# Kernel tuning notes

Measured on AMD Instinct MI355X. Metric: run time of the kernel, lower is better.

Reference implementation:

```python
import jax, jax.numpy as jnp
import numpy as np

N_NODES = 50000
N_EDGES = 800000
N_GRAPHS = 128
IN_DIM = 12          # state_ndim + action_ndim
C = 64               # n_channels
N_LAYERS = 2
NEG_SLOPE = 0.01     # torch leaky_relu default


def setup_inputs() -> dict:
    key = jax.random.key(0)
    ks = jax.random.split(key, 16)
    state = jax.random.normal(ks[0], (N_NODES, 8), dtype=jnp.float32)
    action = jax.random.normal(ks[1], (N_NODES, 4), dtype=jnp.float32)
    edge_index = jax.random.randint(ks[2], (2, N_EDGES), 0, N_NODES, dtype=jnp.int64)
    edge_attr = jax.random.normal(ks[3], (N_EDGES, IN_DIM), dtype=jnp.float32)
    batch = jnp.sort(jax.random.randint(ks[4], (N_NODES,), 0, N_GRAPHS, dtype=jnp.int64))
    s = 0.05
    params = {
        "W_in": jax.random.normal(ks[5], (IN_DIM, C), dtype=jnp.float32) * s,
        "b_in": jnp.zeros((C,), dtype=jnp.float32),
        "W_self": jax.random.normal(ks[6], (N_LAYERS, C, C), dtype=jnp.float32) * s,
        "W_nbr": jax.random.normal(ks[7], (N_LAYERS, C, C), dtype=jnp.float32) * s,
        "W_edge": jax.random.normal(ks[8], (N_LAYERS, IN_DIM, C), dtype=jnp.float32) * s,
        "b_conv": jnp.zeros((N_LAYERS, C), dtype=jnp.float32),
        "W_out": jax.random.normal(ks[9], (C, 1), dtype=jnp.float32) * s,
        "b_out": jnp.zeros((1,), dtype=jnp.float32),
    }
    return {"state": state, "action": action, "edge_index": edge_index,
            "edge_attr": edge_attr, "batch": batch, **params}


def reference(state, action, edge_index, edge_attr, batch,
              W_in, b_in, W_self, W_nbr, W_edge, b_conv, W_out, b_out):
    N = state.shape[0]
    src, dst = edge_index[0], edge_index[1]
    act = lambda v: jax.nn.leaky_relu(v, NEG_SLOPE)

    # read-in: concat state/action -> node embedding [N, C]
    x = jnp.concatenate([state, action], axis=-1)
    h = act(x @ W_in + b_in)

    # message passing: gather -> transform -> scatter-add, edge_attr-conditioned
    for l in range(W_self.shape[0]):
        m = h[src] @ W_nbr[l] + edge_attr @ W_edge[l]          # [E, C]
        agg = jax.ops.segment_sum(m, dst, num_segments=N)      # [N, C]
        h = act(h @ W_self[l] + agg + b_conv[l])

    # read-out to scalar per node, then scatter_mean over graph ids
    y = h @ W_out + b_out                                      # [N, 1]
    sums = jax.ops.segment_sum(y, batch, num_segments=N_GRAPHS)
    counts = jax.ops.segment_sum(jnp.ones((N, 1), y.dtype), batch,
                                 num_segments=N_GRAPHS)
    return sums / jnp.maximum(counts, 1.0)                     # [B, 1]
```

## Files before the change

kernel.cpp:

```cpp
#include <hip/hip_runtime.h>

#define NN 50000
#define NE 800000
#define NG 128
#define IN_DIM 12
#define C 64
#define NEG_SLOPE 0.01f
#define SCAN_BLOCKS 196

typedef short short8 __attribute__((ext_vector_type(8)));
typedef float f32x4 __attribute__((ext_vector_type(4)));
typedef unsigned int uint4v __attribute__((ext_vector_type(4)));

__device__ __forceinline__ float lrelu(float v) {
    return v > 0.f ? v : NEG_SLOPE * v;
}
__device__ __forceinline__ float bflo(uint32_t v) { return __uint_as_float(v << 16); }
__device__ __forceinline__ float bfhi(uint32_t v) { return __uint_as_float(v & 0xffff0000u); }
__device__ __forceinline__ unsigned short bf16r(float x) {
    uint32_t u = __float_as_uint(x);
    u += 0x7fffu + ((u >> 16) & 1u);
    return (unsigned short)(u >> 16);
}
__device__ __forceinline__ uint32_t pack_bf16(float lo, float hi) {
    return (uint32_t)bf16r(lo) | ((uint32_t)bf16r(hi) << 16);
}

__global__ void readin_kernel(const float* __restrict__ state,
                              const float* __restrict__ action,
                              const float* __restrict__ W_in,
                              const float* __restrict__ b_in,
                              uint32_t* __restrict__ hb) {
    __shared__ float sW[IN_DIM * C];
    __shared__ float sb[C];
    int tid = threadIdx.x;
    for (int i = tid; i < IN_DIM * C; i += blockDim.x) sW[i] = W_in[i];
    if (tid < C) sb[tid] = b_in[tid];
    __syncthreads();

    int node = blockIdx.x * (blockDim.x >> 6) + (tid >> 6);
    int c = tid & 63;
    if (node >= NN) return;

    float x[IN_DIM];
#pragma unroll
    for (int k = 0; k < 8; k++) x[k] = state[node * 8 + k];
#pragma unroll
    for (int k = 0; k < 4; k++) x[8 + k] = action[node * 4 + k];

    float acc = sb[c];
#pragma unroll
    for (int k = 0; k < IN_DIM; k++) acc += x[k] * sW[k * C + c];
    float res = lrelu(acc);
    float p = __shfl_xor(res, 1);
    if (!(c & 1)) hb[node * 32 + (c >> 1)] = pack_bf16(res, p);
}

__global__ void hist_kernel(const int* __restrict__ dst, int* __restrict__ deg) {
    int e = blockIdx.x * blockDim.x + threadIdx.x;
    if (e < NE) atomicAdd(&deg[dst[e]], 1);
}

__global__ void scan1_kernel(const int* __restrict__ deg,
                             int* __restrict__ excl,
                             int* __restrict__ bsum) {
    __shared__ int tmp[256];
    int tid = threadIdx.x;
    int i = blockIdx.x * 256 + tid;
    int v = (i < NN) ? deg[i] : 0;
    tmp[tid] = v;
    __syncthreads();
    for (int off = 1; off < 256; off <<= 1) {
        int t = (tid >= off) ? tmp[tid - off] : 0;
        __syncthreads();
        tmp[tid] += t;
        __syncthreads();
    }
    if (i < NN) excl[i] = tmp[tid] - v;
    if (tid == 255) bsum[blockIdx.x] = tmp[255];
}

__global__ void scan23_kernel(const int* __restrict__ excl,
                              const int* __restrict__ bsum,
                              int* __restrict__ row_start,
                              int* __restrict__ cursor) {
    __shared__ int s_off;
    int tid = threadIdx.x;
    if (tid < 64) {
        int p = 0;
        for (int i = tid; i < blockIdx.x; i += 64) p += bsum[i];
#pragma unroll
        for (int off = 32; off; off >>= 1) p += __shfl_xor(p, off);
        if (tid == 0) s_off = p;
    }
    __syncthreads();
    int i = blockIdx.x * 256 + tid;
    if (i < NN) {
        int v = excl[i] + s_off;
        row_start[i] = v;
        cursor[i] = v;
    }
}

__global__ void fill_kernel(const int* __restrict__ src,
                            const int* __restrict__ dst,
                            int* __restrict__ cursor,
                            int* __restrict__ csr_src,
                            int* __restrict__ csr_eid) {
    int e = blockIdx.x * blockDim.x + threadIdx.x;
    if (e >= NE) return;
    int d = dst[e];
    int slot = atomicAdd(&cursor[d], 1);
    csr_src[slot] = src[e];
    csr_eid[slot] = e;
}

__global__ void wprep_kernel(const float* __restrict__ W_self,
                             const float* __restrict__ W_nbr,
                             unsigned short* __restrict__ WT) {
    int idx = blockIdx.x * 256 + threadIdx.x;
    if (idx >= 2 * 64 * 128) return;
    int l = idx >> 13;
    int rem = idx & 8191;
    int col = rem >> 7;
    int k = rem & 127;
    float v = (k < C) ? W_self[l * C * C + k * C + col]
                      : W_nbr[l * C * C + (k - C) * C + col];
    WT[idx] = bf16r(v);
}

__global__ void agg_e_kernel(const float* __restrict__ edge_attr,
                             const int* __restrict__ row_start,
                             const int* __restrict__ deg,
                             const int* __restrict__ csr_eid,
                             const float* __restrict__ W_edge,
                             const float* __restrict__ b_conv,
                             float* __restrict__ E0,
                             float* __restrict__ E1) {
    __shared__ float sWe0[IN_DIM * C];
    __shared__ float sWe1[IN_DIM * C];
    __shared__ float sb0[C];
    __shared__ float sb1[C];
    int tid = threadIdx.x;
    for (int i = tid; i < IN_DIM * C; i += blockDim.x) {
        sWe0[i] = W_edge[i];
        sWe1[i] = W_edge[IN_DIM * C + i];
    }
    if (tid < C) { sb0[tid] = b_conv[tid]; sb1[tid] = b_conv[C + tid]; }
    __syncthreads();

    int node = blockIdx.x * (blockDim.x >> 6) + (tid >> 6);
    int lane = tid & 63;
    int g = lane >> 4;
    int cc = lane & 15;
    if (node >= NN) return;
    int start = row_start[node], cnt = deg[node];

    int myeid = (lane < cnt) ? csr_eid[start + lane] : 0;
    int nb = cnt < 64 ? cnt : 64;

    float acc = 0.f, acc2 = 0.f;
    int j = 0;
    for (; j + 8 <= nb; j += 8) {
        int e0 = __shfl(myeid, j + g);
        int e1 = __shfl(myeid, j + 4 + g);
        if (cc < IN_DIM) {
            acc  += edge_attr[e0 * IN_DIM + cc];
            acc2 += edge_attr[e1 * IN_DIM + cc];
        }
    }
    for (; j + 4 <= nb; j += 4) {
        int e0 = __shfl(myeid, j + g);
        if (cc < IN_DIM) acc += edge_attr[e0 * IN_DIM + cc];
    }
    {
        int e0 = __shfl(myeid, (j + g < 64) ? (j + g) : 0);
        if (j + g < nb && cc < IN_DIM) acc += edge_attr[e0 * IN_DIM + cc];
    }
    for (int i2 = 64 + g; i2 < cnt; i2 += 4) {
        int e = csr_eid[start + i2];
        if (cc < IN_DIM) acc += edge_attr[e * IN_DIM + cc];
    }
    acc += acc2;
    acc += __shfl_xor(acc, 16);
    acc += __shfl_xor(acc, 32);
    float e0v = sb0[lane];
    float e1v = sb1[lane];
#pragma unroll
    for (int k = 0; k < IN_DIM; k++) {
        float ak = __shfl(acc, k);
        e0v += ak * sWe0[k * C + lane];
        e1v += ak * sWe1[k * C + lane];
    }
    E0[node * C + lane] = e0v;
    E1[node * C + lane] = e1v;
}

__global__ void gather_kernel(const uint32_t* __restrict__ hb_in,
                              const int* __restrict__ row_start,
                              const int* __restrict__ deg,
                              const int* __restrict__ csr_src,
                              uint32_t* __restrict__ aggb) {
    int tid = threadIdx.x;
    int node = blockIdx.x * (blockDim.x >> 6) + (tid >> 6);
    int lane = tid & 63;
    if (node >= NN) return;

    int start = row_start[node], cnt = deg[node];
    int half = lane >> 5;
    int q = lane & 31;

    int myidx = (lane < cnt) ? csr_src[start + lane] : 0;
    int nb = cnt < 64 ? cnt : 64;

    float a0 = 0.f, a1 = 0.f, b0v = 0.f, b1v = 0.f;
    int j = 0;
    for (; j + 8 <= nb; j += 8) {
        int p = j + 4 * half;
        int s0 = __shfl(myidx, p);
        int s1 = __shfl(myidx, p + 1);
        int s2 = __shfl(myidx, p + 2);
        int s3 = __shfl(myidx, p + 3);
        uint32_t v0 = hb_in[s0 * 32 + q];
        uint32_t v1 = hb_in[s1 * 32 + q];
        uint32_t v2 = hb_in[s2 * 32 + q];
        uint32_t v3 = hb_in[s3 * 32 + q];
        a0  += bflo(v0); a1  += bfhi(v0);
        b0v += bflo(v1); b1v += bfhi(v1);
        a0  += bflo(v2); a1  += bfhi(v2);
        b0v += bflo(v3); b1v += bfhi(v3);
    }
    for (; j + 2 <= nb; j += 2) {
        int s = __shfl(myidx, j + half);
        uint32_t v = hb_in[s * 32 + q];
        a0 += bflo(v); a1 += bfhi(v);
    }
    {
        int s = __shfl(myidx, (j < 64) ? j : 0);
        if (j < nb && half == 0) {
            uint32_t v = hb_in[s * 32 + q];
            a0 += bflo(v); a1 += bfhi(v);
        }
    }
    for (int i2 = 64 + half; i2 < cnt; i2 += 2) {
        int s = csr_src[start + i2];
        uint32_t v = hb_in[s * 32 + q];
        a0 += bflo(v); a1 += bfhi(v);
    }
    a0 += b0v; a1 += b1v;
    a0 += __shfl_xor(a0, 32);
    a1 += __shfl_xor(a1, 32);
    if (lane < 32) aggb[node * 32 + q] = pack_bf16(a0, a1);
}

__global__ __launch_bounds__(512) void gemm_kernel(
        const uint32_t* __restrict__ hbA,
        const uint32_t* __restrict__ aggb,
        const unsigned short* __restrict__ WT,
        const float* __restrict__ E,
        unsigned short* __restrict__ hb_out) {
    int tid = threadIdx.x;
    int w = tid >> 6;
    int l = tid & 63;
    int mt = blockIdx.x * 2 + (w >> 2);
    if (mt * 16 >= NN) return;
    int nt = w & 3;
    int node_base = mt * 16;

    int arow = l & 15;
    int kg = l >> 4;
    int gcol = nt * 16 + arow;

    const uint32_t* aptr = hbA + (node_base + arow) * 32 + kg * 4;
    const uint32_t* gptr = aggb + (node_base + arow) * 32 + kg * 4;
    short8 a0 = __builtin_bit_cast(short8, *reinterpret_cast<const uint4v*>(aptr));
    short8 a1 = __builtin_bit_cast(short8, *reinterpret_cast<const uint4v*>(aptr + 16));
    short8 a2 = __builtin_bit_cast(short8, *reinterpret_cast<const uint4v*>(gptr));
    short8 a3 = __builtin_bit_cast(short8, *reinterpret_cast<const uint4v*>(gptr + 16));

    const unsigned short* bbase = WT + gcol * 128 + kg * 8;
    short8 b0 = __builtin_bit_cast(short8, *reinterpret_cast<const uint4v*>(bbase));
    short8 b1 = __builtin_bit_cast(short8, *reinterpret_cast<const uint4v*>(bbase + 32));
    short8 b2 = __builtin_bit_cast(short8, *reinterpret_cast<const uint4v*>(bbase + 64));
    short8 b3 = __builtin_bit_cast(short8, *reinterpret_cast<const uint4v*>(bbase + 96));

    f32x4 acc;
#pragma unroll
    for (int r = 0; r < 4; r++)
        acc[r] = E[(node_base + kg * 4 + r) * C + gcol];

    acc = __builtin_amdgcn_mfma_f32_16x16x32_bf16(a0, b0, acc, 0, 0, 0);
    acc = __builtin_amdgcn_mfma_f32_16x16x32_bf16(a1, b1, acc, 0, 0, 0);
    acc = __builtin_amdgcn_mfma_f32_16x16x32_bf16(a2, b2, acc, 0, 0, 0);
    acc = __builtin_amdgcn_mfma_f32_16x16x32_bf16(a3, b3, acc, 0, 0, 0);

#pragma unroll
    for (int r = 0; r < 4; r++) {
        float res = lrelu(acc[r]);
        hb_out[(node_base + kg * 4 + r) * C + gcol] = bf16r(res);
    }
}

__global__ void readout_fused(const unsigned short* __restrict__ hb,
                              const float* __restrict__ W_out,
                              const float* __restrict__ b_out,
                              const int* __restrict__ batch,
                              float* __restrict__ sums,
                              float* __restrict__ counts) {
    __shared__ float s_sum[NG];
    __shared__ float s_cnt[NG];
    int tid = threadIdx.x;
    if (tid < NG) { s_sum[tid] = 0.f; s_cnt[tid] = 0.f; }
    __syncthreads();

    int lane = tid & 63;
    int wave = tid >> 6;
    int base = blockIdx.x * 256 + wave * 64;
    float w = W_out[lane];
    float b0 = b_out[0];

    if (base < NN) {
        int last = base + 63;
        bool full = (last < NN);
        int gf = batch[base];
        int gl = batch[full ? last : (NN - 1)];
        if (full && gf == gl) {
            float p = 0.f;
            for (int i = 0; i < 64; i++)
                p += __uint_as_float((uint32_t)hb[(base + i) * C + lane] << 16);
            p *= w;
#pragma unroll
            for (int off = 32; off; off >>= 1) p += __shfl_xor(p, off);
            if (lane == 0) {
                atomicAdd(&s_sum[gf], p + 64.f * b0);
                atomicAdd(&s_cnt[gf], 64.f);
            }
        } else {
            float y_local = 0.f;
            for (int i = 0; i < 64; i++) {
                int nd = base + i;
                float v = 0.f;
                if (nd < NN) v = __uint_as_float((uint32_t)hb[nd * C + lane] << 16) * w;
#pragma unroll
                for (int off = 32; off; off >>= 1) v += __shfl_xor(v, off);
                if (lane == i) y_local = v + b0;
            }
            int nd = base + lane;
            if (nd < NN) {
                int g = batch[nd];
                atomicAdd(&s_sum[g], y_local);
                atomicAdd(&s_cnt[g], 1.0f);
            }
        }
    }
    __syncthreads();
    if (tid < NG && s_cnt[tid] != 0.f) {
        atomicAdd(&sums[tid], s_sum[tid]);
        atomicAdd(&counts[tid], s_cnt[tid]);
    }
}

__global__ void finalize_kernel(const float* __restrict__ sums,
                                const float* __restrict__ counts,
                                float* __restrict__ out) {
    int g = threadIdx.x;
    if (g < NG) out[g] = sums[g] / fmaxf(counts[g], 1.0f);
}

extern "C" void kernel_launch(void* const* d_in, const int* in_sizes, int n_in,
                              void* d_out, int out_size, void* d_ws, size_t ws_size,
                              hipStream_t stream) {
    const float* state     = (const float*)d_in[0];
    const float* action    = (const float*)d_in[1];
    const int*   edge_index= (const int*)d_in[2];
    const float* edge_attr = (const float*)d_in[3];
    const int*   batch     = (const int*)d_in[4];
    const float* W_in      = (const float*)d_in[5];
    const float* b_in      = (const float*)d_in[6];
    const float* W_self    = (const float*)d_in[7];
    const float* W_nbr     = (const float*)d_in[8];
    const float* W_edge    = (const float*)d_in[9];
    const float* b_conv    = (const float*)d_in[10];
    const float* W_out     = (const float*)d_in[11];
    const float* b_out     = (const float*)d_in[12];
    float* out = (float*)d_out;

    const int* src = edge_index;
    const int* dst = edge_index + NE;

    float* ws      = (float*)d_ws;
    float* E0      = ws;
    float* E1      = E0 + NN * C;
    float* sums    = E1 + NN * C;
    float* counts  = sums + NG;
    int*   deg     = (int*)(counts + NG);
    int*   excl    = deg + NN;
    int*   row_start = excl + NN;
    int*   cursor  = row_start + NN;
    int*   bsum    = cursor + NN;
    int*   csr_src = bsum + 256;
    int*   csr_eid = csr_src + NE;
    uint32_t* hb_a = (uint32_t*)(csr_eid + NE);
    uint32_t* hb_b = hb_a + NN * 32;
    uint32_t* aggb = hb_b + NN * 32;
    unsigned short* WT = (unsigned short*)(aggb + NN * 32);

    hipMemsetAsync(deg, 0, NN * sizeof(int), stream);
    hipMemsetAsync(sums, 0, 2 * NG * sizeof(float), stream);

    const int THREADS = 256;
    int node_blocks = (NN + 3) / 4;
    int edge_tblocks = (NE + THREADS - 1) / THREADS;

    readin_kernel<<<node_blocks, THREADS, 0, stream>>>(state, action, W_in, b_in, hb_a);

    hist_kernel<<<edge_tblocks, THREADS, 0, stream>>>(dst, deg);
    scan1_kernel<<<SCAN_BLOCKS, 256, 0, stream>>>(deg, excl, bsum);
    scan23_kernel<<<SCAN_BLOCKS, 256, 0, stream>>>(excl, bsum, row_start, cursor);
    fill_kernel<<<edge_tblocks, THREADS, 0, stream>>>(src, dst, cursor, csr_src, csr_eid);

    wprep_kernel<<<64, 256, 0, stream>>>(W_self, W_nbr, WT);

    agg_e_kernel<<<node_blocks, THREADS, 0, stream>>>(
        edge_attr, row_start, deg, csr_eid, W_edge, b_conv, E0, E1);

    int gemm_blocks = (3125 + 1) / 2;

    gather_kernel<<<node_blocks, THREADS, 0, stream>>>(hb_a, row_start, deg, csr_src, aggb);
    gemm_kernel<<<gemm_blocks, 512, 0, stream>>>(
        hb_a, aggb, WT, E0, (unsigned short*)hb_b);

    gather_kernel<<<node_blocks, THREADS, 0, stream>>>(hb_b, row_start, deg, csr_src, aggb);
    gemm_kernel<<<gemm_blocks, 512, 0, stream>>>(
        hb_b, aggb, WT + 64 * 128, E1, (unsigned short*)hb_a);

    int ro_blocks = (NN + 255) / 256;
    readout_fused<<<ro_blocks, THREADS, 0, stream>>>(
        (const unsigned short*)hb_a, W_out, b_out, batch, sums, counts);
    finalize_kernel<<<1, 128, 0, stream>>>(sums, counts, out);
}
```

Baseline: 348.5 us.

## Partition CSR build atomics by destination range, interleave CSR arrays, widen gather unroll

The histogram and fill kernels now run 8 owner blocks per edge stripe. Each block only does atomics for destinations inside its node range, which localizes atomic traffic (likely to one XCD's cache given the blockIdx interleave) at the cost of reading dst eight times. The CSR src and edge-id arrays are merged into a single int2 array, so the fill kernel issues one 8-byte store. The gather loop adds a 16-neighbor unrolled path with four accumulator pairs, giving more loads in flight.

After: 338.2 us. 2.9% less time.

```diff
diff --git a/kernel.cpp b/kernel.cpp
--- a/kernel.cpp
+++ b/kernel.cpp
@@ -7,6 +7,10 @@
 #define C 64
 #define NEG_SLOPE 0.01f
 #define SCAN_BLOCKS 196
+#define NOWN 8
+#define OWN_RANGE 6250
+#define ESTRIPE 2048
+#define NSTRIPES ((NE + ESTRIPE - 1) / ESTRIPE)
 
 typedef short short8 __attribute__((ext_vector_type(8)));
 typedef float f32x4 __attribute__((ext_vector_type(4)));
@@ -56,9 +60,16 @@
     if (!(c & 1)) hb[node * 32 + (c >> 1)] = pack_bf16(res, p);
 }
 
-__global__ void hist_kernel(const int* __restrict__ dst, int* __restrict__ deg) {
-    int e = blockIdx.x * blockDim.x + threadIdx.x;
-    if (e < NE) atomicAdd(&deg[dst[e]], 1);
+__global__ void hist_part(const int* __restrict__ dst, int* __restrict__ deg) {
+    int owner = blockIdx.x & (NOWN - 1);
+    int stripe = blockIdx.x >> 3;
+    int lo = owner * OWN_RANGE, hi = lo + OWN_RANGE;
+    int base = stripe * ESTRIPE;
+    int end = base + ESTRIPE; if (end > NE) end = NE;
+    for (int e = base + threadIdx.x; e < end; e += 256) {
+        int d = dst[e];
+        if (d >= lo && d < hi) atomicAdd(&deg[d], 1);
+    }
 }
 
 __global__ void scan1_kernel(const int* __restrict__ deg,
@@ -102,17 +113,22 @@
     }
 }
 
-__global__ void fill_kernel(const int* __restrict__ src,
-                            const int* __restrict__ dst,
-                            int* __restrict__ cursor,
-                            int* __restrict__ csr_src,
-                            int* __restrict__ csr_eid) {
-    int e = blockIdx.x * blockDim.x + threadIdx.x;
-    if (e >= NE) return;
-    int d = dst[e];
-    int slot = atomicAdd(&cursor[d], 1);
-    csr_src[slot] = src[e];
-    csr_eid[slot] = e;
+__global__ void fill_part(const int* __restrict__ src,
+                          const int* __restrict__ dst,
+                          int* __restrict__ cursor,
+                          int2* __restrict__ csr2) {
+    int owner = blockIdx.x & (NOWN - 1);
+    int stripe = blockIdx.x >> 3;
+    int lo = owner * OWN_RANGE, hi = lo + OWN_RANGE;
+    int base = stripe * ESTRIPE;
+    int end = base + ESTRIPE; if (end > NE) end = NE;
+    for (int e = base + threadIdx.x; e < end; e += 256) {
+        int d = dst[e];
+        if (d >= lo && d < hi) {
+            int slot = atomicAdd(&cursor[d], 1);
+            csr2[slot] = make_int2(src[e], e);
+        }
+    }
 }
 
 __global__ void wprep_kernel(const float* __restrict__ W_self,
@@ -132,7 +148,7 @@
 __global__ void agg_e_kernel(const float* __restrict__ edge_attr,
                              const int* __restrict__ row_start,
                              const int* __restrict__ deg,
-                             const int* __restrict__ csr_eid,
+                             const int2* __restrict__ csr2,
                              const float* __restrict__ W_edge,
                              const float* __restrict__ b_conv,
                              float* __restrict__ E0,
@@ -156,7 +172,7 @@
     if (node >= NN) return;
     int start = row_start[node], cnt = deg[node];
 
-    int myeid = (lane < cnt) ? csr_eid[start + lane] : 0;
+    int myeid = (lane < cnt) ? csr2[start + lane].y : 0;
     int nb = cnt < 64 ? cnt : 64;
 
     float acc = 0.f, acc2 = 0.f;
@@ -178,7 +194,7 @@
         if (j + g < nb && cc < IN_DIM) acc += edge_attr[e0 * IN_DIM + cc];
     }
     for (int i2 = 64 + g; i2 < cnt; i2 += 4) {
-        int e = csr_eid[start + i2];
+        int e = csr2[start + i2].y;
         if (cc < IN_DIM) acc += edge_attr[e * IN_DIM + cc];
     }
     acc += acc2;
@@ -199,7 +215,7 @@
 __global__ void gather_kernel(const uint32_t* __restrict__ hb_in,
                               const int* __restrict__ row_start,
                               const int* __restrict__ deg,
-                              const int* __restrict__ csr_src,
+                              const int2* __restrict__ csr2,
                               uint32_t* __restrict__ aggb) {
     int tid = threadIdx.x;
     int node = blockIdx.x * (blockDim.x >> 6) + (tid >> 6);
@@ -210,11 +226,39 @@
     int half = lane >> 5;
     int q = lane & 31;
 
-    int myidx = (lane < cnt) ? csr_src[start + lane] : 0;
+    int myidx = (lane < cnt) ? csr2[start + lane].x : 0;
     int nb = cnt < 64 ? cnt : 64;
 
     float a0 = 0.f, a1 = 0.f, b0v = 0.f, b1v = 0.f;
+    float c0 = 0.f, c1 = 0.f, d0 = 0.f, d1 = 0.f;
     int j = 0;
+    for (; j + 16 <= nb; j += 16) {
+        int p = j + 4 * half;
+        int s0 = __shfl(myidx, p);
+        int s1 = __shfl(myidx, p + 1);
+        int s2 = __shfl(myidx, p + 2);
+        int s3 = __shfl(myidx, p + 3);
+        int s4 = __shfl(myidx, p + 8);
+        int s5 = __shfl(myidx, p + 9);
+        int s6 = __shfl(myidx, p + 10);
+        int s7 = __shfl(myidx, p + 11);
+        uint32_t v0 = hb_in[s0 * 32 + q];
+        uint32_t v1 = hb_in[s1 * 32 + q];
+        uint32_t v2 = hb_in[s2 * 32 + q];
+        uint32_t v3 = hb_in[s3 * 32 + q];
+        uint32_t v4 = hb_in[s4 * 32 + q];
+        uint32_t v5 = hb_in[s5 * 32 + q];
+        uint32_t v6 = hb_in[s6 * 32 + q];
+        uint32_t v7 = hb_in[s7 * 32 + q];
+        a0  += bflo(v0); a1  += bfhi(v0);
+        b0v += bflo(v1); b1v += bfhi(v1);
+        c0  += bflo(v2); c1  += bfhi(v2);
+        d0  += bflo(v3); d1  += bfhi(v3);
+        a0  += bflo(v4); a1  += bfhi(v4);
+        b0v += bflo(v5); b1v += bfhi(v5);
+        c0  += bflo(v6); c1  += bfhi(v6);
+        d0  += bflo(v7); d1  += bfhi(v7);
+    }
     for (; j + 8 <= nb; j += 8) {
         int p = j + 4 * half;
         int s0 = __shfl(myidx, p);
@@ -227,8 +271,8 @@
         uint32_t v3 = hb_in[s3 * 32 + q];
         a0  += bflo(v0); a1  += bfhi(v0);
         b0v += bflo(v1); b1v += bfhi(v1);
-        a0  += bflo(v2); a1  += bfhi(v2);
-        b0v += bflo(v3); b1v += bfhi(v3);
+        c0  += bflo(v2); c1  += bfhi(v2);
+        d0  += bflo(v3); d1  += bfhi(v3);
     }
     for (; j + 2 <= nb; j += 2) {
         int s = __shfl(myidx, j + half);
@@ -243,11 +287,12 @@
         }
     }
     for (int i2 = 64 + half; i2 < cnt; i2 += 2) {
-        int s = csr_src[start + i2];
+        int s = csr2[start + i2].x;
         uint32_t v = hb_in[s * 32 + q];
         a0 += bflo(v); a1 += bfhi(v);
     }
-    a0 += b0v; a1 += b1v;
+    a0 += b0v + c0 + d0;
+    a1 += b1v + c1 + d1;
     a0 += __shfl_xor(a0, 32);
     a1 += __shfl_xor(a1, 32);
     if (lane < 32) aggb[node * 32 + q] = pack_bf16(a0, a1);
@@ -398,9 +443,8 @@
     int*   row_start = excl + NN;
     int*   cursor  = row_start + NN;
     int*   bsum    = cursor + NN;
-    int*   csr_src = bsum + 256;
-    int*   csr_eid = csr_src + NE;
-    uint32_t* hb_a = (uint32_t*)(csr_eid + NE);
+    int2*  csr2    = (int2*)(bsum + 256);
+    uint32_t* hb_a = (uint32_t*)(csr2 + NE);
     uint32_t* hb_b = hb_a + NN * 32;
     uint32_t* aggb = hb_b + NN * 32;
     unsigned short* WT = (unsigned short*)(aggb + NN * 32);
@@ -410,27 +454,27 @@
 
     const int THREADS = 256;
     int node_blocks = (NN + 3) / 4;
-    int edge_tblocks = (NE + THREADS - 1) / THREADS;
+    int part_blocks = NSTRIPES * NOWN;
 
     readin_kernel<<<node_blocks, THREADS, 0, stream>>>(state, action, W_in, b_in, hb_a);
 
-    hist_kernel<<<edge_tblocks, THREADS, 0, stream>>>(dst, deg);
+    hist_part<<<part_blocks, THREADS, 0, stream>>>(dst, deg);
     scan1_kernel<<<SCAN_BLOCKS, 256, 0, stream>>>(deg, excl, bsum);
     scan23_kernel<<<SCAN_BLOCKS, 256, 0, stream>>>(excl, bsum, row_start, cursor);
-    fill_kernel<<<edge_tblocks, THREADS, 0, stream>>>(src, dst, cursor, csr_src, csr_eid);
+    fill_part<<<part_blocks, THREADS, 0, stream>>>(src, dst, cursor, csr2);
 
     wprep_kernel<<<64, 256, 0, stream>>>(W_self, W_nbr, WT);
 
     agg_e_kernel<<<node_blocks, THREADS, 0, stream>>>(
-        edge_attr, row_start, deg, csr_eid, W_edge, b_conv, E0, E1);
+        edge_attr, row_start, deg, csr2, W_edge, b_conv, E0, E1);
 
     int gemm_blocks = (3125 + 1) / 2;
 
-    gather_kernel<<<node_blocks, THREADS, 0, stream>>>(hb_a, row_start, deg, csr_src, aggb);
+    gather_kernel<<<node_blocks, THREADS, 0, stream>>>(hb_a, row_start, deg, csr2, aggb);
     gemm_kernel<<<gemm_blocks, 512, 0, stream>>>(
         hb_a, aggb, WT, E0, (unsigned short*)hb_b);
 
-    gather_kernel<<<node_blocks, THREADS, 0, stream>>>(hb_b, row_start, deg, csr_src, aggb);
+    gather_kernel<<<node_blocks, THREADS, 0, stream>>>(hb_b, row_start, deg, csr2, aggb);
     gemm_kernel<<<gemm_blocks, 512, 0, stream>>>(
         hb_b, aggb, WT + 64 * 128, E1, (unsigned short*)hb_a);
 
```
